# Kernel tuning notes

Measured on AMD Instinct MI355X. Metric: run time of the kernel, lower is better.

## Reference

```python
import jax, jax.numpy as jnp
import numpy as np

N = 64      # hippo_n (state size)
H = 512     # input_size (channels)
L = 2048    # sequence_length


def _hippo_dplr(n):
    # make_HiPPO -> make_NPLR_HiPPO -> make_DPLR_HiPPO (numpy, deterministic)
    pr = np.sqrt(1 + 2 * np.arange(n))
    a = pr[:, None] * pr[None, :]
    a = np.tril(a) - np.diag(np.arange(n))
    a = -a
    p = np.sqrt(np.arange(n) + 0.5)
    b = np.sqrt(2 * np.arange(n) + 1.0)
    s = a + p[:, None] * p[None, :]
    s_diag = np.diagonal(s)
    lam_real = np.mean(s_diag) * np.ones_like(s_diag)
    lam_imag, v = np.linalg.eigh(s * -1j)
    p = v.conj().T @ p
    b = v.conj().T @ b
    return lam_real, lam_imag, p, b


def setup_inputs() -> dict:
    key = jax.random.key(0)
    k_u, k_c, k_step = jax.random.split(key, 3)
    lam_r, lam_i, p, b = _hippo_dplr(N)
    tile = lambda x: jnp.tile(jnp.asarray(x, dtype=jnp.float32), (H, 1))
    dt_min, dt_max = 0.001, 0.1
    log_step = jax.random.uniform(k_step, (H, 1)) * (
        jnp.log(dt_max) - jnp.log(dt_min)) + jnp.log(dt_min)
    return {
        "u": jax.random.normal(k_u, (L, H), dtype=jnp.float32),
        "lambda_real": tile(lam_r),
        "lambda_imag": tile(lam_i),
        "p_real": tile(p.real),
        "p_imag": tile(p.imag),
        "b_real": tile(b.real),
        "b_imag": tile(b.imag),
        "c": jax.random.normal(k_c, (H, N, 2), dtype=jnp.float32) * 0.5 ** 0.5,
        "d": jnp.ones((H, 1), dtype=jnp.float32),
        "log_step": log_step.astype(jnp.float32),
    }


def _s4_convolve(u, lambda_real, lambda_imag, p_real, p_imag,
                 b_real, b_imag, c, d, log_step):
    # u: (L, H); params: (H, N) / (H, N, 2) / (H, 1)
    lam = jnp.clip(lambda_real, None, -0.0001) + 1j * lambda_imag   # (H, N)
    pc = p_real + 1j * p_imag                                        # (H, N)
    bc = b_real + 1j * b_imag                                        # (H, N)
    cc = (c[..., 0] + 1j * c[..., 1]).conj()                         # aterm[0]
    qc = pc.conj()                                                   # aterm[1]
    step = jnp.exp(log_step)                                         # (H, 1)

    Ls = u.shape[0]
    omega = jnp.exp(-2j * jnp.pi * (jnp.arange(Ls) / Ls))            # (L,)
    g = (2.0 / step) * ((1.0 - omega) / (1.0 + omega))[None, :]      # (H, L)
    c2 = 2.0 / (1.0 + omega)                                         # (L,)

    # Shared Cauchy denominator: (H, L, N)
    denom = 1.0 / (g[:, :, None] - lam[:, None, :])
    k00 = jnp.einsum("hn,hln->hl", cc * bc, denom)
    k01 = jnp.einsum("hn,hln->hl", cc * pc, denom)
    k10 = jnp.einsum("hn,hln->hl", qc * bc, denom)
    k11 = jnp.einsum("hn,hln->hl", qc * pc, denom)
    roots = c2[None, :] * (k00 - k01 * (1.0 / (1.0 + k11)) * k10)    # (H, L)
    kern = jnp.fft.ifft(roots, Ls, axis=-1).real                     # (H, L)

    # FFT convolution (fft=True path)
    uT = u.T                                                         # (H, L)
    ud = jnp.fft.rfft(jnp.pad(uT, ((0, 0), (0, Ls))), axis=-1)
    Kd = jnp.fft.rfft(jnp.pad(kern, ((0, 0), (0, Ls))), axis=-1)
    conv = jnp.fft.irfft(ud * Kd, axis=-1)[:, :Ls]                   # (H, L)
    return (conv + d * uT).T                                         # (L, H)


def reference(u, lambda_real, lambda_imag, p_real, p_imag,
              b_real, b_imag, c, d, log_step):
    return _s4_convolve(u, lambda_real, lambda_imag, p_real, p_imag,
                        b_real, b_imag, c, d, log_step)
```

## Files before the change

### kernel.cpp

```cpp
#include <hip/hip_runtime.h>
#include <math.h>

#define L_SEQ 2048
#define H_CH  512
#define N_ST  64
#define BLK   512

__device__ __forceinline__ float frcp(float x) { return __builtin_amdgcn_rcpf(x); }
#define A2(i) ((i) + ((i) >> 4))

template<int LOGN, int ST0 = 0>
__device__ __forceinline__ void fft_lds(float2* buf, const float2* tw,
                                        int tid, float ssign)
{
    constexpr int N   = 1 << LOGN;
    constexpr int NBF = (N / 2) / BLK;
#pragma unroll
    for (int st = ST0; st < LOGN; ++st) {
        const int h2s = (N >> 1) >> st;
#pragma unroll
        for (int bq = 0; bq < NBF; ++bq) {
            const int b  = tid + bq * BLK;
            const int j  = b & (h2s - 1);
            const int i0 = ((b >> (LOGN - 1 - st)) << (LOGN - st)) + j;
            const int i1 = i0 + h2s;
            const float2 uu = buf[A2(i0)];
            const float2 vv = buf[A2(i1)];
            const float2 w  = tw[A2((j << st) << (11 - LOGN))];
            const float  wy = ssign * w.y;
            buf[A2(i0)] = make_float2(uu.x + vv.x, uu.y + vv.y);
            const float d0 = uu.x - vv.x, d1 = uu.y - vv.y;
            buf[A2(i1)] = make_float2(d0 * w.x - d1 * wy, d0 * wy + d1 * w.x);
        }
        __syncthreads();
    }
}

__global__ __launch_bounds__(256)
void s4_prep(const float* __restrict__ lam_r_g, const float* __restrict__ lam_i_g,
             const float* __restrict__ p_r_g,  const float* __restrict__ p_i_g,
             const float* __restrict__ b_r_g,  const float* __restrict__ b_i_g,
             const float* __restrict__ c_g,
             float4* __restrict__ Wa, float4* __restrict__ Wb, float* __restrict__ Wc)
{
    const int g = blockIdx.x * 256 + threadIdx.x;
    const float lr = fminf(lam_r_g[g], -0.0001f);
    const float li = lam_i_g[g];
    const float pr = p_r_g[g], pi = p_i_g[g];
    const float br = b_r_g[g], bi = b_i_g[g];
    const float c0 = c_g[2 * g], c1 = c_g[2 * g + 1];
    Wa[g] = make_float4(lr, li, c0 * br + c1 * bi, c0 * bi - c1 * br);
    Wb[g] = make_float4(c0 * pr + c1 * pi, c0 * pi - c1 * pr,
                        pr * br + pi * bi, pr * bi - pi * br);
    Wc[g] = pr * pr + pi * pi;
}

__global__ __launch_bounds__(BLK)
void s4_fftconv(const float4* __restrict__ Wa, const float4* __restrict__ Wb,
                const float* __restrict__ Wc, const float* __restrict__ log_step_g,
                const float* __restrict__ u, float* __restrict__ Y)
{
    __shared__ float2 bufK[2175];
    __shared__ float2 bufU[2175];
    __shared__ float2 tw[1087];
    const int h   = blockIdx.x;
    const int tid = threadIdx.x;
    float2* __restrict__ rbuf = bufU;

    float uv[4];
#pragma unroll
    for (int q = 0; q < 2; ++q) {
        const int t = tid + q * BLK;
        uv[q]     = u[t * H_CH + h];
        uv[q + 2] = u[(t + 1024) * H_CH + h];
    }

#pragma unroll
    for (int q = 0; q < 2; ++q) {
        const int k = tid + q * BLK;
        float sv, cv;
        sincosf((float)k * (6.2831853071795864769f / 2048.0f), &sv, &cv);
        tw[A2(k)] = make_float2(cv, sv);
    }

    const float step = expf(log_step_g[h]);
    const float ts   = 2.0f / step;
    const float4* __restrict__ wa = Wa + h * N_ST;
    const float4* __restrict__ wb = Wb + h * N_ST;
    const float*  __restrict__ wc = Wc + h * N_ST;

    {
        float grq[4], giq[4], c2rq[4], c2iq[4];
#pragma unroll
        for (int q = 0; q < 4; ++q) {
            const int l = tid + q * BLK;
            float wi, wr;
            sincosf(-6.2831853071795864769f * ((float)l * (1.0f / (float)L_SEQ)),
                    &wi, &wr);
            const float dr = 1.0f + wr, di = wi;
            const float dv = frcp(dr * dr + di * di);
            const float nr = 1.0f - wr, ni = -wi;
            grq[q]  = ts * (nr * dr + ni * di) * dv;
            giq[q]  = ts * (ni * dr - nr * di) * dv;
            c2rq[q] = 2.0f * dr * dv;
            c2iq[q] = -2.0f * di * dv;
        }
        float s00r[4] = {0,0,0,0}, s00i[4] = {0,0,0,0};
        float s01r[4] = {0,0,0,0}, s01i[4] = {0,0,0,0};
        float s10r[4] = {0,0,0,0}, s10i[4] = {0,0,0,0};
        float s11r[4] = {0,0,0,0}, s11i[4] = {0,0,0,0};
#pragma unroll 4
        for (int n = 0; n < N_ST; ++n) {
            const float4 A = wa[n];
            const float4 B = wb[n];
            const float w11 = wc[n];
#pragma unroll
            for (int q = 0; q < 4; ++q) {
                const float ddr = grq[q] - A.x;
                const float ddi = giq[q] - A.y;
                const float rinv = frcp(fmaf(ddr, ddr, ddi * ddi));
                const float rr = ddr * rinv;
                const float ri = -ddi * rinv;
                s00r[q] = fmaf(A.z, rr, fmaf(-A.w, ri, s00r[q]));
                s00i[q] = fmaf(A.z, ri, fmaf( A.w, rr, s00i[q]));
                s01r[q] = fmaf(B.x, rr, fmaf(-B.y, ri, s01r[q]));
                s01i[q] = fmaf(B.x, ri, fmaf( B.y, rr, s01i[q]));
                s10r[q] = fmaf(B.z, rr, fmaf(-B.w, ri, s10r[q]));
                s10i[q] = fmaf(B.z, ri, fmaf( B.w, rr, s10i[q]));
                s11r[q] = fmaf(w11, rr, s11r[q]);
                s11i[q] = fmaf(w11, ri, s11i[q]);
            }
        }
#pragma unroll
        for (int q = 0; q < 4; ++q) {
            const float qdr = 1.0f + s11r[q], qdi = s11i[q];
            const float qinv = frcp(qdr * qdr + qdi * qdi);
            const float pnr = s01r[q] * s10r[q] - s01i[q] * s10i[q];
            const float pni = s01r[q] * s10i[q] + s01i[q] * s10r[q];
            const float qr = (pnr * qdr + pni * qdi) * qinv;
            const float qi = (pni * qdr - pnr * qdi) * qinv;
            const float rr0 = s00r[q] - qr, ri0 = s00i[q] - qi;
            rbuf[tid + q * BLK] =
                make_float2(c2rq[q] * rr0 - c2iq[q] * ri0,
                            c2rq[q] * ri0 + c2iq[q] * rr0);
        }
    }

    __syncthreads();

#pragma unroll
    for (int q = 0; q < 2; ++q) {
        const int k = tid + q * BLK;
        float zr, zi;
        if (k == 0) {
            const float X0 = rbuf[0].x, XM = rbuf[1024].x;
            zr = X0 + XM;  zi = X0 - XM;
        } else {
            const float2 a  = rbuf[k],        b2 = rbuf[2048 - k];
            const float2 a2 = rbuf[1024 - k], b3 = rbuf[1024 + k];
            const float xkr = 0.5f * (a.x + b2.x),  xki = 0.5f * (a.y - b2.y);
            const float xmr = 0.5f * (a2.x + b3.x), xmi = -0.5f * (a2.y - b3.y);
            const float er = xkr + xmr, ei = xki + xmi;
            const float o_r = xkr - xmr, o_i = xki - xmi;
            const float2 w = tw[A2(k)];
            zr = er - fmaf(w.x, o_i,  w.y * o_r);
            zi = ei + fmaf(w.x, o_r, -w.y * o_i);
        }
        bufK[A2(k)] = make_float2(zr, zi);
    }
    __syncthreads();
    fft_lds<10>(bufK, tw, tid, 1.0f);

    float2 v0[2];
#pragma unroll
    for (int q = 0; q < 2; ++q) {
        const int t  = tid + q * BLK;
        const int n0 = t >> 1;
        const float2 za = bufK[A2(__brev(n0) >> 22)];
        const float2 zb = bufK[A2(__brev(512 + n0) >> 22)];
        const float k0v = ((t & 1) ? za.y : za.x) * (1.0f / 2048.0f);
        const float k1v = ((t & 1) ? zb.y : zb.x) * (1.0f / 2048.0f);
        v0[q] = make_float2(k0v, k1v);
    }
    __syncthreads();
#pragma unroll
    for (int q = 0; q < 2; ++q) {
        const int t = tid + q * BLK;
        const float2 v = v0[q];
        const float2 w = tw[A2(t)];
        bufK[A2(t)] = v;
        bufK[A2(t + 1024)] = make_float2(fmaf(v.x, w.x,  v.y * w.y),
                                         fmaf(v.y, w.x, -v.x * w.y));
    }
    __syncthreads();
    fft_lds<11, 1>(bufK, tw, tid, -1.0f);

#pragma unroll
    for (int q = 0; q < 2; ++q) {
        const int t = tid + q * BLK;
        const float2 v = make_float2(uv[q], uv[q + 2]);
        const float2 w = tw[A2(t)];
        bufU[A2(t)] = v;
        bufU[A2(t + 1024)] = make_float2(fmaf(v.x, w.x,  v.y * w.y),
                                         fmaf(v.y, w.x, -v.x * w.y));
    }
    __syncthreads();
    fft_lds<11, 1>(bufU, tw, tid, -1.0f);

    float2 R[4];
#pragma unroll
    for (int q = 0; q < 4; ++q) {
        const int m  = tid + q * BLK;
        const int mp = (2048 - m) & 2047;
        const int bm = __brev(m)  >> 21;
        const int bp = __brev(mp) >> 21;
        const float2 Zk  = bufK[A2(bm)], Zkp = bufK[A2(bp)];
        const float2 Zu  = bufU[A2(bm)], Zup = bufU[A2(bp)];
        const float F0r = 0.5f * (Zk.x + Zkp.x), F0i = 0.5f * (Zk.y - Zkp.y);
        const float F1r = 0.5f * (Zk.y + Zkp.y), F1i = 0.5f * (Zkp.x - Zk.x);
        const float U0r = 0.5f * (Zu.x + Zup.x), U0i = 0.5f * (Zu.y - Zup.y);
        const float U1r = 0.5f * (Zu.y + Zup.y), U1i = 0.5f * (Zup.x - Zu.x);
        const float Pr = F0r * U0r - F0i * U0i;
        const float Pi = F0r * U0i + F0i * U0r;
        const float Qr = F0r * U1r - F0i * U1i + F1r * U0r - F1i * U0i;
        const float Qi = F0r * U1i + F0i * U1r + F1r * U0i + F1i * U0r;
        R[q] = make_float2(Pr - Qi, Pi + Qr);
    }
    __syncthreads();
#pragma unroll
    for (int q = 0; q < 4; ++q) bufK[A2(tid + q * BLK)] = R[q];
    __syncthreads();
    fft_lds<11>(bufK, tw, tid, 1.0f);

#pragma unroll
    for (int q = 0; q < 2; ++q) {
        const int t = tid + q * BLK;
        const float2 rl = bufK[A2(__brev(t)        >> 21)];
        const float2 rh = bufK[A2(__brev(t + 1024) >> 21)];
        Y[h * 2048 + t]        = rl.x * (1.0f / 2048.0f);
        Y[h * 2048 + 1024 + t] = (rh.x + rl.y) * (1.0f / 2048.0f);
    }
}

__global__ __launch_bounds__(256)
void s4_finish(const float* __restrict__ Y, const float* __restrict__ u,
               const float* __restrict__ dvec, float* __restrict__ out)
{
    __shared__ float tile[64][65];
    const int t0   = blockIdx.x * 64;
    const int h0   = blockIdx.y * 64;
    const int lane = threadIdx.x & 63;
    const int rowg = threadIdx.x >> 6;

#pragma unroll
    for (int rr = 0; rr < 16; ++rr) {
        const int hr = rowg * 16 + rr;
        tile[hr][lane] = Y[(h0 + hr) * 2048 + t0 + lane];
    }
    __syncthreads();

    const float dh = dvec[h0 + lane];
#pragma unroll
    for (int rr = 0; rr < 16; ++rr) {
        const int tr = rowg * 16 + rr;
        const int t  = t0 + tr;
        out[t * H_CH + h0 + lane] =
            fmaf(dh, u[t * H_CH + h0 + lane], tile[lane][tr]);
    }
}

extern "C" void kernel_launch(void* const* d_in, const int* in_sizes, int n_in,
                              void* d_out, int out_size, void* d_ws, size_t ws_size,
                              hipStream_t stream)
{
    const float* u        = (const float*)d_in[0];
    const float* lam_r    = (const float*)d_in[1];
    const float* lam_i    = (const float*)d_in[2];
    const float* p_r      = (const float*)d_in[3];
    const float* p_i      = (const float*)d_in[4];
    const float* b_r      = (const float*)d_in[5];
    const float* b_i      = (const float*)d_in[6];
    const float* cmat     = (const float*)d_in[7];
    const float* dvec     = (const float*)d_in[8];
    const float* log_step = (const float*)d_in[9];
    float* out = (float*)d_out;

    char* ws = (char*)d_ws;
    float*  Y     = (float*)(ws + (size_t)8 * 1024 * 1024);
    float4* Wa    = (float4*)(ws + (size_t)12 * 1024 * 1024);
    float4* Wb    = (float4*)(ws + (size_t)12 * 1024 * 1024 + 512 * 1024);
    float*  Wc    = (float*) (ws + (size_t)13 * 1024 * 1024);

    s4_prep<<<dim3(H_CH * N_ST / 256), dim3(256), 0, stream>>>(
        lam_r, lam_i, p_r, p_i, b_r, b_i, cmat, Wa, Wb, Wc);
    s4_fftconv<<<dim3(H_CH), dim3(BLK), 0, stream>>>(
        Wa, Wb, Wc, log_step, u, Y);
    s4_finish<<<dim3(L_SEQ / 64, H_CH / 64), dim3(256), 0, stream>>>(
        Y, u, dvec, out);
}
```

Before: 61.86 us.

## Use radix-4 LDS FFT stages and run the kernel and input FFTs together

Replaces the radix-2 shared-memory FFT with a radix-4 form that fuses two stages per pass, halving the number of barrier-separated passes and LDS round trips. The kernel and input forward FFTs are also merged into one dual-buffer loop that shares twiddle loads and barriers. The cost is more registers per thread and fewer independent butterflies per thread for the smaller FFTs, which could hurt occupancy or leave threads idle.

```diff
diff --git a/kernel.cpp b/kernel.cpp
--- a/kernel.cpp
+++ b/kernel.cpp
@@ -9,28 +9,89 @@
 __device__ __forceinline__ float frcp(float x) { return __builtin_amdgcn_rcpf(x); }
 #define A2(i) ((i) + ((i) >> 4))
 
+__device__ __forceinline__ void quad_bfly(float2* __restrict__ buf,
+                                          const float2 w1, const float2 w2,
+                                          float S, int e00, int e01, int e10, int e11)
+{
+    const float2 u0 = buf[e00], u1 = buf[e01];
+    const float2 v0 = buf[e10], v1 = buf[e11];
+    const float w1y = S * w1.y, w2y = S * w2.y;
+    const float2 A = make_float2(u0.x + v0.x, u0.y + v0.y);
+    const float2 C = make_float2(u1.x + v1.x, u1.y + v1.y);
+    float dx = u0.x - v0.x, dy = u0.y - v0.y;
+    const float2 B  = make_float2(dx * w1.x - dy * w1y, dx * w1y + dy * w1.x);
+    dx = u1.x - v1.x;  dy = u1.y - v1.y;
+    const float2 Dc = make_float2(dx * w1.x - dy * w1y, dx * w1y + dy * w1.x);
+    const float2 D  = make_float2(-S * Dc.y, S * Dc.x);
+    buf[e00] = make_float2(A.x + C.x, A.y + C.y);
+    dx = A.x - C.x;  dy = A.y - C.y;
+    buf[e01] = make_float2(dx * w2.x - dy * w2y, dx * w2y + dy * w2.x);
+    buf[e10] = make_float2(B.x + D.x, B.y + D.y);
+    dx = B.x - D.x;  dy = B.y - D.y;
+    buf[e11] = make_float2(dx * w2.x - dy * w2y, dx * w2y + dy * w2.x);
+}
+
 template<int LOGN, int ST0 = 0>
-__device__ __forceinline__ void fft_lds(float2* buf, const float2* tw,
-                                        int tid, float ssign)
-{
-    constexpr int N   = 1 << LOGN;
-    constexpr int NBF = (N / 2) / BLK;
-#pragma unroll
-    for (int st = ST0; st < LOGN; ++st) {
-        const int h2s = (N >> 1) >> st;
-#pragma unroll
-        for (int bq = 0; bq < NBF; ++bq) {
-            const int b  = tid + bq * BLK;
-            const int j  = b & (h2s - 1);
-            const int i0 = ((b >> (LOGN - 1 - st)) << (LOGN - st)) + j;
-            const int i1 = i0 + h2s;
+__device__ __forceinline__ void fft4_lds(float2* buf, const float2* tw,
+                                         int tid, float ssign)
+{
+    constexpr int N  = 1 << LOGN;
+    constexpr int SH = 11 - LOGN;
+    int st = ST0;
+    if constexpr (((LOGN - ST0) & 1) != 0) {
+        const int H = (N >> 1) >> ST0;
+        for (int b = tid; b < N / 2; b += BLK) {
+            const int j  = b & (H - 1);
+            const int i0 = ((b >> (LOGN - 1 - ST0)) << (LOGN - ST0)) + j;
+            const int i1 = i0 + H;
             const float2 uu = buf[A2(i0)];
             const float2 vv = buf[A2(i1)];
-            const float2 w  = tw[A2((j << st) << (11 - LOGN))];
+            const float2 w  = tw[A2((j << ST0) << SH)];
             const float  wy = ssign * w.y;
             buf[A2(i0)] = make_float2(uu.x + vv.x, uu.y + vv.y);
             const float d0 = uu.x - vv.x, d1 = uu.y - vv.y;
             buf[A2(i1)] = make_float2(d0 * w.x - d1 * wy, d0 * wy + d1 * w.x);
+        }
+        __syncthreads();
+        st = ST0 + 1;
+    }
+    for (; st < LOGN; st += 2) {
+        const int H  = (N >> 1) >> st;
+        const int HQ = H >> 1;
+        for (int q = tid; q < N / 4; q += BLK) {
+            const int j   = q & (HQ - 1);
+            const int blk = q >> (LOGN - 2 - st);
+            const int i0  = (blk << (LOGN - st)) + j;
+            quad_bfly(buf,
+                      tw[A2((j << st) << SH)],
+                      tw[A2((j << (st + 1)) << SH)],
+                      ssign,
+                      A2(i0), A2(i0 + HQ), A2(i0 + H), A2(i0 + H + HQ));
+        }
+        __syncthreads();
+    }
+}
+
+template<int LOGN, int ST0>
+__device__ __forceinline__ void fft4_lds_dual(float2* bK, float2* bU,
+                                              const float2* tw, int tid, float ssign)
+{
+    constexpr int N  = 1 << LOGN;
+    constexpr int SH = 11 - LOGN;
+    static_assert(((LOGN - ST0) & 1) == 0, "dual needs even stage count");
+    for (int st = ST0; st < LOGN; st += 2) {
+        const int H  = (N >> 1) >> st;
+        const int HQ = H >> 1;
+        for (int q = tid; q < N / 4; q += BLK) {
+            const int j   = q & (HQ - 1);
+            const int blk = q >> (LOGN - 2 - st);
+            const int i0  = (blk << (LOGN - st)) + j;
+            const float2 w1 = tw[A2((j << st) << SH)];
+            const float2 w2 = tw[A2((j << (st + 1)) << SH)];
+            const int e00 = A2(i0), e01 = A2(i0 + HQ);
+            const int e10 = A2(i0 + H), e11 = A2(i0 + H + HQ);
+            quad_bfly(bK, w1, w2, ssign, e00, e01, e10, e11);
+            quad_bfly(bU, w1, w2, ssign, e00, e01, e10, e11);
         }
         __syncthreads();
     }
@@ -169,7 +230,7 @@
         bufK[A2(k)] = make_float2(zr, zi);
     }
     __syncthreads();
-    fft_lds<10>(bufK, tw, tid, 1.0f);
+    fft4_lds<10>(bufK, tw, tid, 1.0f);
 
     float2 v0[2];
 #pragma unroll
@@ -186,26 +247,18 @@
 #pragma unroll
     for (int q = 0; q < 2; ++q) {
         const int t = tid + q * BLK;
-        const float2 v = v0[q];
         const float2 w = tw[A2(t)];
-        bufK[A2(t)] = v;
-        bufK[A2(t + 1024)] = make_float2(fmaf(v.x, w.x,  v.y * w.y),
-                                         fmaf(v.y, w.x, -v.x * w.y));
-    }
-    __syncthreads();
-    fft_lds<11, 1>(bufK, tw, tid, -1.0f);
-
-#pragma unroll
-    for (int q = 0; q < 2; ++q) {
-        const int t = tid + q * BLK;
-        const float2 v = make_float2(uv[q], uv[q + 2]);
-        const float2 w = tw[A2(t)];
-        bufU[A2(t)] = v;
-        bufU[A2(t + 1024)] = make_float2(fmaf(v.x, w.x,  v.y * w.y),
-                                         fmaf(v.y, w.x, -v.x * w.y));
-    }
-    __syncthreads();
-    fft_lds<11, 1>(bufU, tw, tid, -1.0f);
+        const float2 vk = v0[q];
+        bufK[A2(t)] = vk;
+        bufK[A2(t + 1024)] = make_float2(fmaf(vk.x, w.x,  vk.y * w.y),
+                                         fmaf(vk.y, w.x, -vk.x * w.y));
+        const float2 vu = make_float2(uv[q], uv[q + 2]);
+        bufU[A2(t)] = vu;
+        bufU[A2(t + 1024)] = make_float2(fmaf(vu.x, w.x,  vu.y * w.y),
+                                         fmaf(vu.y, w.x, -vu.x * w.y));
+    }
+    __syncthreads();
+    fft4_lds_dual<11, 1>(bufK, bufU, tw, tid, -1.0f);
 
     float2 R[4];
 #pragma unroll
@@ -230,7 +283,7 @@
 #pragma unroll
     for (int q = 0; q < 4; ++q) bufK[A2(tid + q * BLK)] = R[q];
     __syncthreads();
-    fft_lds<11>(bufK, tw, tid, 1.0f);
+    fft4_lds<11>(bufK, tw, tid, 1.0f);
 
 #pragma unroll
     for (int q = 0; q < 2; ++q) {
```

Result: faster. 60.42 us (-2.3%).
